# Kernel tuning notes

Measured on AMD Instinct MI355X. Metric: run time of the kernel, lower is better.

The kernel has to match this reference:

```python
import jax, jax.numpy as jnp
import numpy as np
from jax.scipy.special import logsumexp


def setup_inputs() -> dict:
    key = jax.random.key(0)
    k1, k2, k3, k4 = jax.random.split(key, 4)
    B, n, d = 64, 8192, 1024
    return {
        "query": jax.random.normal(k1, (B, d), dtype=jnp.float32),
        "stored_keys": jax.random.normal(k2, (n, d), dtype=jnp.float32),
        "stored_theta": jax.random.normal(k3, (n, d // 2), dtype=jnp.float32),
        "stored_mag": jax.random.normal(k4, (n, 1), dtype=jnp.float32),
        "top_k": 4,
    }


def reference(query, stored_keys, stored_theta, stored_mag, top_k):
    # scores[b, i] = logsumexp_d(query[b, d] + keys[i, d])  -> [B, n]
    # (query is detached in the original torch code)
    q = jax.lax.stop_gradient(query)
    scores = logsumexp(q[:, None, :] + stored_keys[None, :, :], axis=-1)
    topk_s, topk_i = jax.lax.top_k(scores, top_k)       # [B, k] each
    w = jax.nn.softmax(topk_s, axis=-1)                 # [B, k]
    theta = stored_theta[topk_i]                        # [B, k, d//2]
    mag = stored_mag[topk_i]                            # [B, k, 1]
    return (theta, mag, w)
```

## Files before the change

### kernel.cpp

```cpp
#include <hip/hip_runtime.h>
#include <math.h>

#define N_KEYS 8192
#define DIM    1024
#define BQ     64
#define TOPK   4
#define HD     512
#define KSPLIT 2
#define KSLICE (DIM / KSPLIT)
#define NBLK   32
#define KC     128
#define NCHUNK (KSLICE / KC)

typedef _Float16 half8 __attribute__((ext_vector_type(8)));
typedef _Float16 half4 __attribute__((ext_vector_type(4)));
typedef float    f32x4 __attribute__((ext_vector_type(4)));

__device__ __forceinline__ bool better(float av, int ai, float bv, int bi) {
    return (av > bv) || (av == bv && ai < bi);
}

__device__ __forceinline__ void ce(float& av, int& ai, float& bv, int& bi) {
    if (!better(av, ai, bv, bi)) {
        float tv = av; av = bv; bv = tv;
        int   ti = ai; ai = bi; bi = ti;
    }
}

__device__ __forceinline__ void merge_shfl(float v[4], int ix[4], int off) {
    float pv[4]; int pi[4];
    #pragma unroll
    for (int r = 0; r < 4; ++r) {
        pv[r] = __shfl_xor(v[r], off);
        pi[r] = __shfl_xor(ix[r], off);
    }
    float nv[4]; int ni[4];
    #pragma unroll
    for (int r = 0; r < 4; ++r) {
        bool ta = better(v[r], ix[r], pv[3 - r], pi[3 - r]);
        nv[r] = ta ? v[r]  : pv[3 - r];
        ni[r] = ta ? ix[r] : pi[3 - r];
    }
    ce(nv[0], ni[0], nv[2], ni[2]);
    ce(nv[1], ni[1], nv[3], ni[3]);
    ce(nv[0], ni[0], nv[1], ni[1]);
    ce(nv[2], ni[2], nv[3], ni[3]);
    #pragma unroll
    for (int r = 0; r < 4; ++r) { v[r] = nv[r]; ix[r] = ni[r]; }
}

__global__ __launch_bounds__(256) void prep_q(const float4* __restrict__ q4,
                                              _Float16* __restrict__ eqh,
                                              _Float16* __restrict__ eql) {
    int i = blockIdx.x * 256 + threadIdx.x;
    float4 v = q4[i];
    float e0 = expf(v.x), e1 = expf(v.y), e2 = expf(v.z), e3 = expf(v.w);
    half4 h, l;
    h[0] = (_Float16)e0; h[1] = (_Float16)e1; h[2] = (_Float16)e2; h[3] = (_Float16)e3;
    l[0] = (_Float16)(e0 - (float)h[0]); l[1] = (_Float16)(e1 - (float)h[1]);
    l[2] = (_Float16)(e2 - (float)h[2]); l[3] = (_Float16)(e3 - (float)h[3]);
    *(half4*)&eqh[i * 4] = h;
    *(half4*)&eql[i * 4] = l;
}

__device__ __forceinline__ void stage_write(_Float16* BhB, _Float16* BlB,
                                            int key, int c4, float4 v) {
    float e0 = expf(v.x), e1 = expf(v.y), e2 = expf(v.z), e3 = expf(v.w);
    half4 h, l;
    h[0] = (_Float16)e0; h[1] = (_Float16)e1; h[2] = (_Float16)e2; h[3] = (_Float16)e3;
    l[0] = (_Float16)(e0 - (float)h[0]); l[1] = (_Float16)(e1 - (float)h[1]);
    l[2] = (_Float16)(e2 - (float)h[2]); l[3] = (_Float16)(e3 - (float)h[3]);
    int g   = (c4 >> 1) ^ (key & 7);
    int idx = key * KC + g * 8 + (c4 & 1) * 4;
    *(half4*)(BhB + idx) = h;
    *(half4*)(BlB + idx) = l;
}

__global__ __launch_bounds__(512, 4) void scores_mfma(
        const _Float16* __restrict__ eqh, const _Float16* __restrict__ eql,
        const float* __restrict__ keys, float* __restrict__ part) {
    __shared__ _Float16 Bh[2][NBLK * KC];
    __shared__ _Float16 Bl[2][NBLK * KC];

    const int t    = threadIdx.x;
    const int lane = t & 63, w = t >> 6;
    const int wm   = w >> 1, wn = w & 1;
    const int l15  = lane & 15, l4 = lane >> 4;
    const int i0    = blockIdx.x * NBLK;
    const int dbase = blockIdx.y * KSLICE;

    const int key0 = t >> 5;
    const int c4s  = t & 31;

    const float* kb = keys + (size_t)i0 * DIM + dbase + 4 * c4s;

    float4 p0 = *(const float4*)(kb + (size_t)key0 * DIM);
    float4 p1 = *(const float4*)(kb + (size_t)(key0 + 16) * DIM);
    stage_write(Bh[0], Bl[0], key0,      c4s, p0);
    stage_write(Bh[0], Bl[0], key0 + 16, c4s, p1);
    __syncthreads();

    f32x4 acc = {0.f, 0.f, 0.f, 0.f};
    const int arow = 16 * wm + l15;
    const int kk   = 16 * wn + l15;

    for (int c = 0; c < NCHUNK; ++c) {
        const int buf = c & 1;
        if (c + 1 < NCHUNK) {
            const float* kbc = kb + (c + 1) * KC;
            p0 = *(const float4*)(kbc + (size_t)key0 * DIM);
            p1 = *(const float4*)(kbc + (size_t)(key0 + 16) * DIM);
        }
        #pragma unroll
        for (int ks = 0; ks < KC / 32; ++ks) {
            const _Float16* ap = &eqh[(size_t)arow * DIM + dbase + c * KC + ks * 32 + l4 * 8];
            half8 Ah = *(const half8*)ap;
            half8 Al = *(const half8*)&eql[(size_t)arow * DIM + dbase + c * KC + ks * 32 + l4 * 8];
            int g = ((ks * 4 + l4) ^ (kk & 7)) * 8;
            half8 bh = *(const half8*)&Bh[buf][kk * KC + g];
            half8 bl = *(const half8*)&Bl[buf][kk * KC + g];
            acc = __builtin_amdgcn_mfma_f32_16x16x32_f16(Ah, bh, acc, 0, 0, 0);
            acc = __builtin_amdgcn_mfma_f32_16x16x32_f16(Ah, bl, acc, 0, 0, 0);
            acc = __builtin_amdgcn_mfma_f32_16x16x32_f16(Al, bh, acc, 0, 0, 0);
        }
        if (c + 1 < NCHUNK) {
            stage_write(Bh[buf ^ 1], Bl[buf ^ 1], key0,      c4s, p0);
            stage_write(Bh[buf ^ 1], Bl[buf ^ 1], key0 + 16, c4s, p1);
        }
        __syncthreads();
    }

    float* pb = part + (size_t)blockIdx.y * (BQ * N_KEYS);
    #pragma unroll
    for (int r = 0; r < 4; ++r) {
        int row = 16 * wm + l4 * 4 + r;
        int col = i0 + 16 * wn + l15;
        pb[(size_t)row * N_KEYS + col] = acc[r];
    }
}

template<int KS>
__global__ __launch_bounds__(1024) void topk_partial(const float* __restrict__ part,
                                                     float* __restrict__ cv,
                                                     int* __restrict__ ci) {
    const int b     = blockIdx.x >> 2;
    const int chunk = blockIdx.x & 3;
    const int t     = threadIdx.x;
    const int lane  = t & 63, wid = t >> 6;

    __shared__ float sv[16][4];
    __shared__ int   si[16][4];

    float v[4]  = {-INFINITY, -INFINITY, -INFINITY, -INFINITY};
    int   ix[4] = {0x7fffffff, 0x7fffffff, 0x7fffffff, 0x7fffffff};

    const float* pb = part + (size_t)b * N_KEYS;
    #pragma unroll
    for (int r = 0; r < 2; ++r) {
        int i = chunk * 2048 + t + r * 1024;
        float s = 0.f;
        #pragma unroll
        for (int sl = 0; sl < KS; ++sl)
            s += pb[(size_t)sl * (BQ * N_KEYS) + i];
        if (better(s, i, v[3], ix[3])) {
            v[3] = s; ix[3] = i;
            #pragma unroll
            for (int p = 3; p > 0; --p) {
                if (better(v[p], ix[p], v[p - 1], ix[p - 1])) {
                    float tv = v[p]; v[p] = v[p-1]; v[p-1] = tv;
                    int   ti = ix[p]; ix[p] = ix[p-1]; ix[p-1] = ti;
                }
            }
        }
    }
    merge_shfl(v, ix, 1);  merge_shfl(v, ix, 2);  merge_shfl(v, ix, 4);
    merge_shfl(v, ix, 8);  merge_shfl(v, ix, 16); merge_shfl(v, ix, 32);

    if (lane == 0) {
        #pragma unroll
        for (int r = 0; r < 4; ++r) { sv[wid][r] = v[r]; si[wid][r] = ix[r]; }
    }
    __syncthreads();

    if (wid == 0) {
        float mv[4]; int mi[4];
        if (lane < 16) {
            #pragma unroll
            for (int r = 0; r < 4; ++r) { mv[r] = sv[lane][r]; mi[r] = si[lane][r]; }
        } else {
            #pragma unroll
            for (int r = 0; r < 4; ++r) { mv[r] = -INFINITY; mi[r] = 0x7fffffff; }
        }
        merge_shfl(mv, mi, 1); merge_shfl(mv, mi, 2);
        merge_shfl(mv, mi, 4); merge_shfl(mv, mi, 8);
        if (lane == 0) {
            #pragma unroll
            for (int r = 0; r < 4; ++r) {
                cv[blockIdx.x * 4 + r] = mv[r];
                ci[blockIdx.x * 4 + r] = mi[r];
            }
        }
    }
}

__global__ __launch_bounds__(64) void finalize_kernel(const float* __restrict__ cv,
                                                      const int* __restrict__ ci,
                                                      const float* __restrict__ theta,
                                                      const float* __restrict__ mag,
                                                      float* __restrict__ out) {
    const int b    = blockIdx.x;
    const int lane = threadIdx.x;

    __shared__ float fw[4];
    __shared__ int   fi[4];

    float v[4]  = {-INFINITY, -INFINITY, -INFINITY, -INFINITY};
    int   ix[4] = {0x7fffffff, 0x7fffffff, 0x7fffffff, 0x7fffffff};
    if (lane < 4) {
        #pragma unroll
        for (int r = 0; r < 4; ++r) {
            v[r]  = cv[(b * 4 + lane) * 4 + r];
            ix[r] = ci[(b * 4 + lane) * 4 + r];
        }
    }
    merge_shfl(v, ix, 1); merge_shfl(v, ix, 2);

    if (lane == 0) {
        float ssum = v[0] + v[1] + v[2] + v[3];
        #pragma unroll
        for (int r = 0; r < 4; ++r) { fw[r] = v[r] / ssum; fi[r] = ix[r]; }
    }
    __syncthreads();

    const float4* th4 = (const float4*)theta;
    float4* out4 = (float4*)out;
    #pragma unroll
    for (int r = 0; r < 8; ++r) {
        int l = lane + r * 64;
        int j = l >> 7, c4 = l & 127;
        out4[((size_t)b * TOPK + j) * (HD / 4) + c4] = th4[(size_t)fi[j] * (HD / 4) + c4];
    }
    if (lane < TOPK) {
        out[(size_t)BQ * TOPK * HD + b * TOPK + lane]             = mag[fi[lane]];
        out[(size_t)BQ * TOPK * HD + BQ * TOPK + b * TOPK + lane] = fw[lane];
    }
}

extern "C" void kernel_launch(void* const* d_in, const int* in_sizes, int n_in,
                              void* d_out, int out_size, void* d_ws, size_t ws_size,
                              hipStream_t stream) {
    const float* q     = (const float*)d_in[0];
    const float* keys  = (const float*)d_in[1];
    const float* theta = (const float*)d_in[2];
    const float* mag   = (const float*)d_in[3];
    float* out = (float*)d_out;

    float*    part = (float*)d_ws;
    _Float16* eqh  = (_Float16*)(part + (size_t)KSPLIT * BQ * N_KEYS);
    _Float16* eql  = eqh + (size_t)BQ * DIM;
    float*    cv   = (float*)(eql + (size_t)BQ * DIM);
    int*      ci   = (int*)(cv + BQ * 4 * TOPK);

    prep_q<<<BQ * DIM / 4 / 256, 256, 0, stream>>>((const float4*)q, eqh, eql);
    scores_mfma<<<dim3(N_KEYS / NBLK, KSPLIT), 512, 0, stream>>>(eqh, eql, keys, part);
    topk_partial<KSPLIT><<<BQ * 4, 1024, 0, stream>>>(part, cv, ci);
    finalize_kernel<<<BQ, 64, 0, stream>>>(cv, ci, theta, mag, out);
}
```

Baseline: 37.79 us.

## Restructure score GEMM: wider K-split, direct global-to-LDS loads, exp in registers

The score kernel now splits the reduction dimension eight ways instead of two and gives each block 64 keys over a 128-wide slice. Each of the four waves loads its own raw fp32 key tile straight into LDS with global_load_lds, using a rotated layout to avoid bank conflicts. The exp and fp16 hi/lo split now happen in registers after reading LDS, replacing the double-buffered exp-then-stage pipeline. Each wave computes all 64 query rows, so A-fragments are loaded once per B-fragment. The cost is a four-times larger partial-score buffer that the top-k kernel must write and then read and sum, and there is no longer any overlap between loads and MFMA inside a block.

```diff
diff --git a/kernel.cpp b/kernel.cpp
--- a/kernel.cpp
+++ b/kernel.cpp
@@ -6,15 +6,19 @@
 #define BQ     64
 #define TOPK   4
 #define HD     512
-#define KSPLIT 2
+#define KSPLIT 8
 #define KSLICE (DIM / KSPLIT)
-#define NBLK   32
-#define KC     128
-#define NCHUNK (KSLICE / KC)
+#define NBLK   64
 
 typedef _Float16 half8 __attribute__((ext_vector_type(8)));
 typedef _Float16 half4 __attribute__((ext_vector_type(4)));
 typedef float    f32x4 __attribute__((ext_vector_type(4)));
+
+#if defined(__has_builtin)
+#if __has_builtin(__builtin_amdgcn_global_load_lds)
+#define HAS_GLLDS 1
+#endif
+#endif
 
 __device__ __forceinline__ bool better(float av, int ai, float bv, int bi) {
     return (av > bv) || (av == bv && ai < bi);
@@ -63,80 +67,73 @@
     *(half4*)&eql[i * 4] = l;
 }
 
-__device__ __forceinline__ void stage_write(_Float16* BhB, _Float16* BlB,
-                                            int key, int c4, float4 v) {
-    float e0 = expf(v.x), e1 = expf(v.y), e2 = expf(v.z), e3 = expf(v.w);
-    half4 h, l;
-    h[0] = (_Float16)e0; h[1] = (_Float16)e1; h[2] = (_Float16)e2; h[3] = (_Float16)e3;
-    l[0] = (_Float16)(e0 - (float)h[0]); l[1] = (_Float16)(e1 - (float)h[1]);
-    l[2] = (_Float16)(e2 - (float)h[2]); l[3] = (_Float16)(e3 - (float)h[3]);
-    int g   = (c4 >> 1) ^ (key & 7);
-    int idx = key * KC + g * 8 + (c4 & 1) * 4;
-    *(half4*)(BhB + idx) = h;
-    *(half4*)(BlB + idx) = l;
-}
-
-__global__ __launch_bounds__(512, 4) void scores_mfma(
+__global__ __launch_bounds__(256, 4) void scores_mfma(
         const _Float16* __restrict__ eqh, const _Float16* __restrict__ eql,
         const float* __restrict__ keys, float* __restrict__ part) {
-    __shared__ _Float16 Bh[2][NBLK * KC];
-    __shared__ _Float16 Bl[2][NBLK * KC];
+    __shared__ float Braw[4 * 16 * 32 * 4];
 
     const int t    = threadIdx.x;
     const int lane = t & 63, w = t >> 6;
-    const int wm   = w >> 1, wn = w & 1;
-    const int l15  = lane & 15, l4 = lane >> 4;
+    const int l15  = lane & 15, l4 = lane >> 4, r7 = lane & 7;
     const int i0    = blockIdx.x * NBLK;
     const int dbase = blockIdx.y * KSLICE;
 
-    const int key0 = t >> 5;
-    const int c4s  = t & 31;
-
-    const float* kb = keys + (size_t)i0 * DIM + dbase + 4 * c4s;
-
-    float4 p0 = *(const float4*)(kb + (size_t)key0 * DIM);
-    float4 p1 = *(const float4*)(kb + (size_t)(key0 + 16) * DIM);
-    stage_write(Bh[0], Bl[0], key0,      c4s, p0);
-    stage_write(Bh[0], Bl[0], key0 + 16, c4s, p1);
-    __syncthreads();
-
-    f32x4 acc = {0.f, 0.f, 0.f, 0.f};
-    const int arow = 16 * wm + l15;
-    const int kk   = 16 * wn + l15;
-
-    for (int c = 0; c < NCHUNK; ++c) {
-        const int buf = c & 1;
-        if (c + 1 < NCHUNK) {
-            const float* kbc = kb + (c + 1) * KC;
-            p0 = *(const float4*)(kbc + (size_t)key0 * DIM);
-            p1 = *(const float4*)(kbc + (size_t)(key0 + 16) * DIM);
-        }
-        #pragma unroll
-        for (int ks = 0; ks < KC / 32; ++ks) {
-            const _Float16* ap = &eqh[(size_t)arow * DIM + dbase + c * KC + ks * 32 + l4 * 8];
-            half8 Ah = *(const half8*)ap;
-            half8 Al = *(const half8*)&eql[(size_t)arow * DIM + dbase + c * KC + ks * 32 + l4 * 8];
-            int g = ((ks * 4 + l4) ^ (kk & 7)) * 8;
-            half8 bh = *(const half8*)&Bh[buf][kk * KC + g];
-            half8 bl = *(const half8*)&Bl[buf][kk * KC + g];
-            acc = __builtin_amdgcn_mfma_f32_16x16x32_f16(Ah, bh, acc, 0, 0, 0);
-            acc = __builtin_amdgcn_mfma_f32_16x16x32_f16(Ah, bl, acc, 0, 0, 0);
-            acc = __builtin_amdgcn_mfma_f32_16x16x32_f16(Al, bh, acc, 0, 0, 0);
-        }
-        if (c + 1 < NCHUNK) {
-            stage_write(Bh[buf ^ 1], Bl[buf ^ 1], key0,      c4s, p0);
-            stage_write(Bh[buf ^ 1], Bl[buf ^ 1], key0 + 16, c4s, p1);
-        }
-        __syncthreads();
-    }
-
-    float* pb = part + (size_t)blockIdx.y * (BQ * N_KEYS);
-    #pragma unroll
-    for (int r = 0; r < 4; ++r) {
-        int row = 16 * wm + l4 * 4 + r;
-        int col = i0 + 16 * wn + l15;
-        pb[(size_t)row * N_KEYS + col] = acc[r];
-    }
+    float* wbase = &Braw[w * 2048];
+
+    #pragma unroll
+    for (int j = 0; j < 8; ++j) {
+        int s   = j * 64 + lane;
+        int row = s >> 5;
+        int p   = s & 31;
+        int g   = (p & 24) | ((p - row) & 7);
+        const float* src = keys + (size_t)(i0 + 16 * w + row) * DIM + dbase + g * 4;
+#ifdef HAS_GLLDS
+        __builtin_amdgcn_global_load_lds(
+            (const __attribute__((address_space(1))) void*)src,
+            (__attribute__((address_space(3))) void*)(wbase + j * 256), 16, 0, 0);
+#else
+        *(float4*)(wbase + s * 4) = *(const float4*)src;
+#endif
+    }
+#ifdef HAS_GLLDS
+    asm volatile("s_waitcnt vmcnt(0)" ::: "memory");
+    __builtin_amdgcn_sched_barrier(0);
+#endif
+
+    f32x4 acc[4] = {};
+
+    #pragma unroll
+    for (int ks = 0; ks < 4; ++ks) {
+        int p0 = ks * 8 + ((2 * l4 + 0 + r7) & 7);
+        int p1 = ks * 8 + ((2 * l4 + 1 + r7) & 7);
+        float4 b0 = *(const float4*)&wbase[l15 * 128 + p0 * 4];
+        float4 b1 = *(const float4*)&wbase[l15 * 128 + p1 * 4];
+        float e[8] = {__expf(b0.x), __expf(b0.y), __expf(b0.z), __expf(b0.w),
+                      __expf(b1.x), __expf(b1.y), __expf(b1.z), __expf(b1.w)};
+        half8 Bh, Bl;
+        #pragma unroll
+        for (int j = 0; j < 8; ++j) {
+            _Float16 h = (_Float16)e[j];
+            Bh[j] = h;
+            Bl[j] = (_Float16)(e[j] - (float)h);
+        }
+        #pragma unroll
+        for (int mt = 0; mt < 4; ++mt) {
+            const size_t aoff = (size_t)(16 * mt + l15) * DIM + dbase + ks * 32 + l4 * 8;
+            half8 Ah = *(const half8*)&eqh[aoff];
+            half8 Al = *(const half8*)&eql[aoff];
+            acc[mt] = __builtin_amdgcn_mfma_f32_16x16x32_f16(Ah, Bh, acc[mt], 0, 0, 0);
+            acc[mt] = __builtin_amdgcn_mfma_f32_16x16x32_f16(Ah, Bl, acc[mt], 0, 0, 0);
+            acc[mt] = __builtin_amdgcn_mfma_f32_16x16x32_f16(Al, Bh, acc[mt], 0, 0, 0);
+        }
+    }
+
+    float* pb = part + (size_t)blockIdx.y * (BQ * N_KEYS) + i0 + 16 * w + l15;
+    #pragma unroll
+    for (int mt = 0; mt < 4; ++mt)
+        #pragma unroll
+        for (int r = 0; r < 4; ++r)
+            pb[(size_t)(16 * mt + l4 * 4 + r) * N_KEYS] = acc[mt][r];
 }
 
 template<int KS>
@@ -262,7 +259,7 @@
     int*      ci   = (int*)(cv + BQ * 4 * TOPK);
 
     prep_q<<<BQ * DIM / 4 / 256, 256, 0, stream>>>((const float4*)q, eqh, eql);
-    scores_mfma<<<dim3(N_KEYS / NBLK, KSPLIT), 512, 0, stream>>>(eqh, eql, keys, part);
+    scores_mfma<<<dim3(N_KEYS / NBLK, KSPLIT), 256, 0, stream>>>(eqh, eql, keys, part);
     topk_partial<KSPLIT><<<BQ * 4, 1024, 0, stream>>>(part, cv, ci);
     finalize_kernel<<<BQ, 64, 0, stream>>>(cv, ci, theta, mag, out);
 }
```

New measurement: 43.60 us. +15.4%, slower.

## Fuse score MFMA with per-block top-k and drop K-split partial scores

Applied to the files above, without the earlier changes.

Replaces the K-split scores kernel plus separate top-k pass with one kernel. Each block handles 16 keys over the full dimension, writes its scores to shared memory, and emits a per-query top-4 candidate list, so the large partial-score buffer is never written or read back. The finalize kernel now merges 512 candidates per query with 256 threads. The change also prefetches query fragments into registers with double buffering, splits the MFMA accumulators into three chains, and uses fast __expf. In exchange the grid is smaller-tiled with fewer rows per block, and the finalize merge is wider.

```diff
diff --git a/kernel.cpp b/kernel.cpp
--- a/kernel.cpp
+++ b/kernel.cpp
@@ -1,16 +1,16 @@
 #include <hip/hip_runtime.h>
 #include <math.h>
 
-#define N_KEYS 8192
-#define DIM    1024
-#define BQ     64
-#define TOPK   4
-#define HD     512
-#define KSPLIT 2
-#define KSLICE (DIM / KSPLIT)
-#define NBLK   32
-#define KC     128
-#define NCHUNK (KSLICE / KC)
+#define N_KEYS  8192
+#define DIM     1024
+#define BQ      64
+#define TOPK    4
+#define HD      512
+#define NBLK    16
+#define NBLOCKS (N_KEYS / NBLK)
+#define CD      128
+#define NCHUNK  (DIM / CD)
+#define SCP     (NBLK + 1)
 
 typedef _Float16 half8 __attribute__((ext_vector_type(8)));
 typedef _Float16 half4 __attribute__((ext_vector_type(4)));
@@ -24,6 +24,19 @@
     if (!better(av, ai, bv, bi)) {
         float tv = av; av = bv; bv = tv;
         int   ti = ai; ai = bi; bi = ti;
+    }
+}
+
+__device__ __forceinline__ void ins4(float v[4], int ix[4], float s, int gi) {
+    if (better(s, gi, v[3], ix[3])) {
+        v[3] = s; ix[3] = gi;
+        #pragma unroll
+        for (int p = 3; p > 0; --p) {
+            if (better(v[p], ix[p], v[p - 1], ix[p - 1])) {
+                float tv = v[p]; v[p] = v[p-1]; v[p-1] = tv;
+                int   ti = ix[p]; ix[p] = ix[p-1]; ix[p-1] = ti;
+            }
+        }
     }
 }
 
@@ -54,7 +67,7 @@
                                               _Float16* __restrict__ eql) {
     int i = blockIdx.x * 256 + threadIdx.x;
     float4 v = q4[i];
-    float e0 = expf(v.x), e1 = expf(v.y), e2 = expf(v.z), e3 = expf(v.w);
+    float e0 = __expf(v.x), e1 = __expf(v.y), e2 = __expf(v.z), e3 = __expf(v.w);
     half4 h, l;
     h[0] = (_Float16)e0; h[1] = (_Float16)e1; h[2] = (_Float16)e2; h[3] = (_Float16)e3;
     l[0] = (_Float16)(e0 - (float)h[0]); l[1] = (_Float16)(e1 - (float)h[1]);
@@ -63,116 +76,142 @@
     *(half4*)&eql[i * 4] = l;
 }
 
-__device__ __forceinline__ void stage_write(_Float16* BhB, _Float16* BlB,
-                                            int key, int c4, float4 v) {
-    float e0 = expf(v.x), e1 = expf(v.y), e2 = expf(v.z), e3 = expf(v.w);
-    half4 h, l;
-    h[0] = (_Float16)e0; h[1] = (_Float16)e1; h[2] = (_Float16)e2; h[3] = (_Float16)e3;
-    l[0] = (_Float16)(e0 - (float)h[0]); l[1] = (_Float16)(e1 - (float)h[1]);
-    l[2] = (_Float16)(e2 - (float)h[2]); l[3] = (_Float16)(e3 - (float)h[3]);
-    int g   = (c4 >> 1) ^ (key & 7);
-    int idx = key * KC + g * 8 + (c4 & 1) * 4;
-    *(half4*)(BhB + idx) = h;
-    *(half4*)(BlB + idx) = l;
-}
-
-__global__ __launch_bounds__(512, 4) void scores_mfma(
+__global__ __launch_bounds__(256, 2) void fused_scores_topk(
         const _Float16* __restrict__ eqh, const _Float16* __restrict__ eql,
-        const float* __restrict__ keys, float* __restrict__ part) {
-    __shared__ _Float16 Bh[2][NBLK * KC];
-    __shared__ _Float16 Bl[2][NBLK * KC];
+        const float* __restrict__ keys,
+        float* __restrict__ cv, int* __restrict__ ci) {
+    __shared__ _Float16 Bh[2][NBLK * CD];
+    __shared__ _Float16 Bl[2][NBLK * CD];
+    __shared__ float sc[BQ * SCP];
 
     const int t    = threadIdx.x;
     const int lane = t & 63, w = t >> 6;
-    const int wm   = w >> 1, wn = w & 1;
     const int l15  = lane & 15, l4 = lane >> 4;
-    const int i0    = blockIdx.x * NBLK;
-    const int dbase = blockIdx.y * KSLICE;
-
-    const int key0 = t >> 5;
-    const int c4s  = t & 31;
-
-    const float* kb = keys + (size_t)i0 * DIM + dbase + 4 * c4s;
-
-    float4 p0 = *(const float4*)(kb + (size_t)key0 * DIM);
-    float4 p1 = *(const float4*)(kb + (size_t)(key0 + 16) * DIM);
-    stage_write(Bh[0], Bl[0], key0,      c4s, p0);
-    stage_write(Bh[0], Bl[0], key0 + 16, c4s, p1);
-    __syncthreads();
-
-    f32x4 acc = {0.f, 0.f, 0.f, 0.f};
-    const int arow = 16 * wm + l15;
-    const int kk   = 16 * wn + l15;
-
+    const int i0   = blockIdx.x * NBLK;
+
+    const int srow = t >> 4, sg = t & 15;
+    const int sgp  = (sg & 8) | ((sg ^ srow) & 7);
+    const float* ksrc = keys + (size_t)(i0 + srow) * DIM + sg * 8;
+
+    const int arow = 16 * w + l15;
+    const _Float16* aph = eqh + (size_t)arow * DIM + l4 * 8;
+    const _Float16* apl = eql + (size_t)arow * DIM + l4 * 8;
+
+    float4 r0, r1;
+    half8 ah[2][4], al[2][4];
+
+#define LOADK(c) do { \
+        const float* s_ = ksrc + (c) * CD; \
+        r0 = *(const float4*)s_; r1 = *(const float4*)(s_ + 4); \
+    } while (0)
+
+#define LOADA(c, pb) do { \
+        _Pragma("unroll") \
+        for (int ks_ = 0; ks_ < 4; ++ks_) { \
+            ah[pb][ks_] = *(const half8*)(aph + (c) * CD + ks_ * 32); \
+            al[pb][ks_] = *(const half8*)(apl + (c) * CD + ks_ * 32); \
+        } \
+    } while (0)
+
+#define WRITEK(buf) do { \
+        float e_[8] = {__expf(r0.x), __expf(r0.y), __expf(r0.z), __expf(r0.w), \
+                       __expf(r1.x), __expf(r1.y), __expf(r1.z), __expf(r1.w)}; \
+        half8 h_, l_; \
+        _Pragma("unroll") \
+        for (int j_ = 0; j_ < 8; ++j_) { \
+            _Float16 hh_ = (_Float16)e_[j_]; \
+            h_[j_] = hh_; \
+            l_[j_] = (_Float16)(e_[j_] - (float)hh_); \
+        } \
+        *(half8*)&Bh[buf][srow * CD + sgp * 8] = h_; \
+        *(half8*)&Bl[buf][srow * CD + sgp * 8] = l_; \
+    } while (0)
+
+    LOADK(0);
+    LOADA(0, 0);
+    WRITEK(0);
+    __syncthreads();
+
+    f32x4 acc0 = {0.f, 0.f, 0.f, 0.f};
+    f32x4 acc1 = {0.f, 0.f, 0.f, 0.f};
+    f32x4 acc2 = {0.f, 0.f, 0.f, 0.f};
+
+    const int rmask = l15 & 7;
+
+    #pragma unroll
     for (int c = 0; c < NCHUNK; ++c) {
         const int buf = c & 1;
         if (c + 1 < NCHUNK) {
-            const float* kbc = kb + (c + 1) * KC;
-            p0 = *(const float4*)(kbc + (size_t)key0 * DIM);
-            p1 = *(const float4*)(kbc + (size_t)(key0 + 16) * DIM);
-        }
-        #pragma unroll
-        for (int ks = 0; ks < KC / 32; ++ks) {
-            const _Float16* ap = &eqh[(size_t)arow * DIM + dbase + c * KC + ks * 32 + l4 * 8];
-            half8 Ah = *(const half8*)ap;
-            half8 Al = *(const half8*)&eql[(size_t)arow * DIM + dbase + c * KC + ks * 32 + l4 * 8];
-            int g = ((ks * 4 + l4) ^ (kk & 7)) * 8;
-            half8 bh = *(const half8*)&Bh[buf][kk * KC + g];
-            half8 bl = *(const half8*)&Bl[buf][kk * KC + g];
-            acc = __builtin_amdgcn_mfma_f32_16x16x32_f16(Ah, bh, acc, 0, 0, 0);
-            acc = __builtin_amdgcn_mfma_f32_16x16x32_f16(Ah, bl, acc, 0, 0, 0);
-            acc = __builtin_amdgcn_mfma_f32_16x16x32_f16(Al, bh, acc, 0, 0, 0);
-        }
-        if (c + 1 < NCHUNK) {
-            stage_write(Bh[buf ^ 1], Bl[buf ^ 1], key0,      c4s, p0);
-            stage_write(Bh[buf ^ 1], Bl[buf ^ 1], key0 + 16, c4s, p1);
-        }
+            LOADK(c + 1);
+            LOADA(c + 1, buf ^ 1);
+        }
+        #pragma unroll
+        for (int ks = 0; ks < 4; ++ks) {
+            int g  = ks * 4 + l4;
+            int gp = (g & 8) | ((g ^ rmask) & 7);
+            half8 bh = *(const half8*)&Bh[buf][l15 * CD + gp * 8];
+            half8 bl = *(const half8*)&Bl[buf][l15 * CD + gp * 8];
+            acc0 = __builtin_amdgcn_mfma_f32_16x16x32_f16(ah[buf][ks], bh, acc0, 0, 0, 0);
+            acc1 = __builtin_amdgcn_mfma_f32_16x16x32_f16(ah[buf][ks], bl, acc1, 0, 0, 0);
+            acc2 = __builtin_amdgcn_mfma_f32_16x16x32_f16(al[buf][ks], bh, acc2, 0, 0, 0);
+        }
+        if (c + 1 < NCHUNK) WRITEK(buf ^ 1);
         __syncthreads();
     }
 
-    float* pb = part + (size_t)blockIdx.y * (BQ * N_KEYS);
-    #pragma unroll
-    for (int r = 0; r < 4; ++r) {
-        int row = 16 * wm + l4 * 4 + r;
-        int col = i0 + 16 * wn + l15;
-        pb[(size_t)row * N_KEYS + col] = acc[r];
-    }
-}
-
-template<int KS>
-__global__ __launch_bounds__(1024) void topk_partial(const float* __restrict__ part,
-                                                     float* __restrict__ cv,
-                                                     int* __restrict__ ci) {
-    const int b     = blockIdx.x >> 2;
-    const int chunk = blockIdx.x & 3;
-    const int t     = threadIdx.x;
-    const int lane  = t & 63, wid = t >> 6;
-
-    __shared__ float sv[16][4];
-    __shared__ int   si[16][4];
-
-    float v[4]  = {-INFINITY, -INFINITY, -INFINITY, -INFINITY};
-    int   ix[4] = {0x7fffffff, 0x7fffffff, 0x7fffffff, 0x7fffffff};
-
-    const float* pb = part + (size_t)b * N_KEYS;
-    #pragma unroll
-    for (int r = 0; r < 2; ++r) {
-        int i = chunk * 2048 + t + r * 1024;
-        float s = 0.f;
-        #pragma unroll
-        for (int sl = 0; sl < KS; ++sl)
-            s += pb[(size_t)sl * (BQ * N_KEYS) + i];
-        if (better(s, i, v[3], ix[3])) {
-            v[3] = s; ix[3] = i;
-            #pragma unroll
-            for (int p = 3; p > 0; --p) {
-                if (better(v[p], ix[p], v[p - 1], ix[p - 1])) {
-                    float tv = v[p]; v[p] = v[p-1]; v[p-1] = tv;
-                    int   ti = ix[p]; ix[p] = ix[p-1]; ix[p-1] = ti;
-                }
-            }
-        }
-    }
+    #pragma unroll
+    for (int r = 0; r < 4; ++r)
+        sc[(16 * w + l4 * 4 + r) * SCP + l15] = acc0[r] + acc1[r] + acc2[r];
+    __syncthreads();
+
+    {
+        const int q = t >> 2, sub = t & 3;
+        float v[4]  = {-INFINITY, -INFINITY, -INFINITY, -INFINITY};
+        int   ix[4] = {0x7fffffff, 0x7fffffff, 0x7fffffff, 0x7fffffff};
+        #pragma unroll
+        for (int j = 0; j < 4; ++j) {
+            int kl = sub * 4 + j;
+            ins4(v, ix, sc[q * SCP + kl], i0 + kl);
+        }
+        merge_shfl(v, ix, 1);
+        merge_shfl(v, ix, 2);
+        if (sub == 0) {
+            float4 vv = make_float4(v[0], v[1], v[2], v[3]);
+            int4   ii = make_int4(ix[0], ix[1], ix[2], ix[3]);
+            ((float4*)cv)[q * NBLOCKS + blockIdx.x] = vv;
+            ((int4*)ci)[q * NBLOCKS + blockIdx.x]   = ii;
+        }
+    }
+#undef LOADK
+#undef LOADA
+#undef WRITEK
+}
+
+__global__ __launch_bounds__(256) void finalize_kernel(
+        const float* __restrict__ cv, const int* __restrict__ ci,
+        const float* __restrict__ theta, const float* __restrict__ mag,
+        float* __restrict__ out) {
+    const int b = blockIdx.x;
+    const int t = threadIdx.x;
+    const int lane = t & 63, wid = t >> 6;
+
+    __shared__ float sv[4][4];
+    __shared__ int   si[4][4];
+    __shared__ float fw[4];
+    __shared__ int   fi[4];
+
+    float4 va = ((const float4*)cv)[b * NBLOCKS + t];
+    int4   ia = ((const int4*)ci)[b * NBLOCKS + t];
+    float4 vb = ((const float4*)cv)[b * NBLOCKS + 256 + t];
+    int4   ib = ((const int4*)ci)[b * NBLOCKS + 256 + t];
+
+    float v[4]  = {va.x, va.y, va.z, va.w};
+    int   ix[4] = {ia.x, ia.y, ia.z, ia.w};
+    ins4(v, ix, vb.x, ib.x);
+    ins4(v, ix, vb.y, ib.y);
+    ins4(v, ix, vb.z, ib.z);
+    ins4(v, ix, vb.w, ib.w);
+
     merge_shfl(v, ix, 1);  merge_shfl(v, ix, 2);  merge_shfl(v, ix, 4);
     merge_shfl(v, ix, 8);  merge_shfl(v, ix, 16); merge_shfl(v, ix, 32);
 
@@ -184,7 +223,7 @@
 
     if (wid == 0) {
         float mv[4]; int mi[4];
-        if (lane < 16) {
+        if (lane < 4) {
             #pragma unroll
             for (int r = 0; r < 4; ++r) { mv[r] = sv[lane][r]; mi[r] = si[lane][r]; }
         } else {
@@ -192,57 +231,25 @@
             for (int r = 0; r < 4; ++r) { mv[r] = -INFINITY; mi[r] = 0x7fffffff; }
         }
         merge_shfl(mv, mi, 1); merge_shfl(mv, mi, 2);
-        merge_shfl(mv, mi, 4); merge_shfl(mv, mi, 8);
         if (lane == 0) {
+            float ssum = mv[0] + mv[1] + mv[2] + mv[3];
             #pragma unroll
-            for (int r = 0; r < 4; ++r) {
-                cv[blockIdx.x * 4 + r] = mv[r];
-                ci[blockIdx.x * 4 + r] = mi[r];
-            }
-        }
-    }
-}
-
-__global__ __launch_bounds__(64) void finalize_kernel(const float* __restrict__ cv,
-                                                      const int* __restrict__ ci,
-                                                      const float* __restrict__ theta,
-                                                      const float* __restrict__ mag,
-                                                      float* __restrict__ out) {
-    const int b    = blockIdx.x;
-    const int lane = threadIdx.x;
-
-    __shared__ float fw[4];
-    __shared__ int   fi[4];
-
-    float v[4]  = {-INFINITY, -INFINITY, -INFINITY, -INFINITY};
-    int   ix[4] = {0x7fffffff, 0x7fffffff, 0x7fffffff, 0x7fffffff};
-    if (lane < 4) {
-        #pragma unroll
-        for (int r = 0; r < 4; ++r) {
-            v[r]  = cv[(b * 4 + lane) * 4 + r];
-            ix[r] = ci[(b * 4 + lane) * 4 + r];
-        }
-    }
-    merge_shfl(v, ix, 1); merge_shfl(v, ix, 2);
-
-    if (lane == 0) {
-        float ssum = v[0] + v[1] + v[2] + v[3];
-        #pragma unroll
-        for (int r = 0; r < 4; ++r) { fw[r] = v[r] / ssum; fi[r] = ix[r]; }
+            for (int r = 0; r < 4; ++r) { fw[r] = mv[r] / ssum; fi[r] = mi[r]; }
+        }
     }
     __syncthreads();
 
     const float4* th4 = (const float4*)theta;
     float4* out4 = (float4*)out;
     #pragma unroll
-    for (int r = 0; r < 8; ++r) {
-        int l = lane + r * 64;
+    for (int r = 0; r < 2; ++r) {
+        int l = t + r * 256;
         int j = l >> 7, c4 = l & 127;
         out4[((size_t)b * TOPK + j) * (HD / 4) + c4] = th4[(size_t)fi[j] * (HD / 4) + c4];
     }
-    if (lane < TOPK) {
-        out[(size_t)BQ * TOPK * HD + b * TOPK + lane]             = mag[fi[lane]];
-        out[(size_t)BQ * TOPK * HD + BQ * TOPK + b * TOPK + lane] = fw[lane];
+    if (t < TOPK) {
+        out[(size_t)BQ * TOPK * HD + b * TOPK + t]             = mag[fi[t]];
+        out[(size_t)BQ * TOPK * HD + BQ * TOPK + b * TOPK + t] = fw[t];
     }
 }
 
@@ -255,14 +262,12 @@
     const float* mag   = (const float*)d_in[3];
     float* out = (float*)d_out;
 
-    float*    part = (float*)d_ws;
-    _Float16* eqh  = (_Float16*)(part + (size_t)KSPLIT * BQ * N_KEYS);
-    _Float16* eql  = eqh + (size_t)BQ * DIM;
-    float*    cv   = (float*)(eql + (size_t)BQ * DIM);
-    int*      ci   = (int*)(cv + BQ * 4 * TOPK);
+    _Float16* eqh = (_Float16*)d_ws;
+    _Float16* eql = eqh + (size_t)BQ * DIM;
+    float*    cv  = (float*)(eql + (size_t)BQ * DIM);
+    int*      ci  = (int*)(cv + (size_t)BQ * NBLOCKS * 4);
 
     prep_q<<<BQ * DIM / 4 / 256, 256, 0, stream>>>((const float4*)q, eqh, eql);
-    scores_mfma<<<dim3(N_KEYS / NBLK, KSPLIT), 512, 0, stream>>>(eqh, eql, keys, part);
-    topk_partial<KSPLIT><<<BQ * 4, 1024, 0, stream>>>(part, cv, ci);
-    finalize_kernel<<<BQ, 64, 0, stream>>>(cv, ci, theta, mag, out);
-}
+    fused_scores_topk<<<NBLOCKS, 256, 0, stream>>>(eqh, eql, keys, cv, ci);
+    finalize_kernel<<<BQ, 256, 0, stream>>>(cv, ci, theta, mag, out);
+}
```

After: 36.09 us. -4.5%, faster.
